# Kernel tuning notes

Measured on AMD Instinct MI355X. Metric: run time of the kernel, lower is better.

Reference implementation:

```python
import jax, jax.numpy as jnp
import numpy as np

B, M, N, HID, H, P = 16, 1024, 1024, 512, 8, 2
DH = HID // H


def setup_inputs() -> dict:
    key = jax.random.key(0)
    k1, k2, k3, k4 = jax.random.split(key, 4)
    X = jax.random.normal(k1, (B, M, HID), dtype=jnp.float32)
    Y = jax.random.normal(k2, (B, N, HID), dtype=jnp.float32)
    # learned pad prefixes (kaiming-uniform in torch; any init is fine for a numerics baseline)
    bound = np.sqrt(1.0 / HID)
    pad_x = jax.random.uniform(k3, (P, HID), dtype=jnp.float32, minval=-bound, maxval=bound)
    pad_y = jax.random.uniform(k4, (P, HID), dtype=jnp.float32, minval=-bound, maxval=bound)
    return {"X": X, "Y": Y, "pad_x": pad_x, "pad_y": pad_y}


def _project(T, pad):
    # prepend learned pad rows, split into heads -> [B, H, L+P, DH]
    b = T.shape[0]
    T = jnp.concatenate([jnp.broadcast_to(pad[None], (b, P, HID)), T], axis=1)
    return T.reshape(b, T.shape[1], H, DH).transpose(0, 2, 1, 3)


def reference(X, Y, pad_x, pad_y):
    Xp = _project(X, pad_x)  # [B,H,Mp,DH], query=key=value
    Yp = _project(Y, pad_y)  # [B,H,Np,DH]
    # shared similarity matrix (no 1/sqrt(d) scaling in the original)
    sim = jnp.einsum('bhmd,bhnd->bhmn', Xp, Yp)  # [B,H,Mp,Np]
    # masks in the original are all-ones (pad rows + torch.ones), so masked_fill is a no-op
    attn_X_by_Y = jax.nn.softmax(sim, axis=2)  # softmax over Mp (rows)
    attn_Y_by_X = jax.nn.softmax(sim, axis=3)  # softmax over Np (cols)
    # X attends in Y: attn^T @ X_value -> [B,H,Np,DH]
    X_in_Y = jnp.einsum('bhmn,bhmd->bhnd', attn_X_by_Y, Xp)[:, :, P:, :]
    X_in_Y = X_in_Y.transpose(0, 2, 1, 3).reshape(X.shape[0], -1, HID)  # [B,N,HID]
    # Y attends in X: attn @ Y_value -> [B,H,Mp,DH]
    Y_in_X = jnp.einsum('bhmn,bhnd->bhmd', attn_Y_by_X, Yp)[:, :, P:, :]
    Y_in_X = Y_in_X.transpose(0, 2, 1, 3).reshape(Y.shape[0], -1, HID)  # [B,M,HID]
    return X_in_Y, Y_in_X
```

## Files before the change

### kernel.cpp

```cpp
#include <hip/hip_runtime.h>
#include <hip/hip_bf16.h>
#include <stdint.h>

typedef _Float16 f16x8_t  __attribute__((ext_vector_type(8)));
typedef float    f32x16_t __attribute__((ext_vector_type(16)));
typedef short    s16x8_t  __attribute__((ext_vector_type(8)));
typedef unsigned uint2v   __attribute__((ext_vector_type(2)));
typedef unsigned int u32;

#define MFMA32 __builtin_amdgcn_mfma_f32_32x32x16_f16

#if __has_builtin(__builtin_amdgcn_exp2f)
#define EXP2(x) __builtin_amdgcn_exp2f(x)
#else
#define EXP2(x) exp2f(x)
#endif

__device__ __forceinline__ u32 PKRTZ(float a, float b) {
    return __builtin_bit_cast(u32, __builtin_amdgcn_cvt_pkrtz(a, b));
}

__device__ __forceinline__ void PLSWAP(u32& a, u32& b) {
#if __has_builtin(__builtin_amdgcn_permlane32_swap)
    uint2v r = __builtin_amdgcn_permlane32_swap(a, b, false, false);
    a = r[0]; b = r[1];
#else
    u32 pa = (u32)__shfl_xor((int)a, 32);
    u32 pb = (u32)__shfl_xor((int)b, 32);
    const int hi_ = (int)((threadIdx.x & 63) >> 5);
    u32 na = hi_ ? pb : a;
    u32 nb = hi_ ? b  : pa;
    a = na; b = nb;
#endif
}
__device__ __forceinline__ float swap_add(float v) {
    u32 a = __builtin_bit_cast(u32, v), b = a;
    PLSWAP(a, b);
    return __builtin_bit_cast(float, a) + __builtin_bit_cast(float, b);
}
__device__ __forceinline__ float swap_max(float v) {
    u32 a = __builtin_bit_cast(u32, v), b = a;
    PLSWAP(a, b);
    return fmaxf(__builtin_bit_cast(float, a), __builtin_bit_cast(float, b));
}

constexpr int Bb   = 16;
constexpr int HIDc = 512;
constexpr int SEQc = 1024;

constexpr int QT = 128;
constexpr int KT = 64;
constexpr int NTILES = SEQc / KT;

constexpr float LOG2E_F = 1.4426950408889634f;
constexpr float DTHR    = 11.5f;

constexpr int ROWB       = 144;
constexpr int VT_OFF     = 64 * ROWB;
constexpr int BUF_STRIDE = 2 * VT_OFF;
constexpr int LDS_TOTAL  = 2 * BUF_STRIDE;

__global__ __launch_bounds__(256, 4)
void xattn_kernel(const float* __restrict__ X, const float* __restrict__ Y,
                  const float* __restrict__ padx, const float* __restrict__ pady,
                  float* __restrict__ out)
{
    __shared__ __align__(16) unsigned char pool[LDS_TOTAL];

    const int tid  = threadIdx.x;
    const int w    = tid >> 6;
    const int lane = tid & 63;
    const int l31  = lane & 31;
    const int hi   = lane >> 5;

    const unsigned hid = blockIdx.x + gridDim.x * (blockIdx.y + gridDim.y * blockIdx.z);
    const unsigned lid = (hid & 7u) * 256u + (hid >> 3);
    const int qt   = lid & 7;
    const int bh   = (lid >> 3) & 127;
    const int pass = lid >> 10;
    const int b    = bh >> 3;
    const int h    = bh & 7;

    const float* Qp   = pass == 0 ? X : Y;
    const float* KVp  = pass == 0 ? Y : X;
    const float* padp = pass == 0 ? pady : padx;
    float* outp = out + (pass == 0 ? (size_t)Bb * SEQc * HIDc : (size_t)0);

    const float* qrow = Qp + ((size_t)b * SEQc + qt * QT + w * 32 + l31) * HIDc + h * 64;
    f16x8_t qf[4];
#pragma unroll
    for (int ds = 0; ds < 4; ++ds) {
        const float* src = qrow + ds * 16 + hi * 8;
        float4 a = *(const float4*)src;
        float4 c = *(const float4*)(src + 4);
        uint4 uu = {PKRTZ(a.x * LOG2E_F, a.y * LOG2E_F), PKRTZ(a.z * LOG2E_F, a.w * LOG2E_F),
                    PKRTZ(c.x * LOG2E_F, c.y * LOG2E_F), PKRTZ(c.z * LOG2E_F, c.w * LOG2E_F)};
        qf[ds] = __builtin_bit_cast(f16x8_t, uu);
    }

    const float* padh = padp + h * 64;
    float s0 = 0.f, s1 = 0.f;
#pragma unroll
    for (int ds = 0; ds < 4; ++ds)
#pragma unroll
        for (int j = 0; j < 8; ++j) {
            float qv = (float)qf[ds][j];
            int d = ds * 16 + hi * 8 + j;
            s0 += qv * padh[d];
            s1 += qv * padh[HIDc + d];
        }
    s0 = swap_add(s0);
    s1 = swap_add(s1);
    float mr = fmaxf(s0, s1);
    float e0 = EXP2(s0 - mr), e1 = EXP2(s1 - mr);
    float lr = e0 + e1;

    f32x16_t Oacc[2];
#pragma unroll
    for (int db = 0; db < 2; ++db)
#pragma unroll
        for (int r = 0; r < 16; ++r) {
            int d = db * 32 + (r & 3) + 8 * (r >> 2) + 4 * hi;
            Oacc[db][r] = e0 * padh[d] + e1 * padh[HIDc + d];
        }

    const unsigned key  = (unsigned)(((l31 >> 3) & 3) << 4);
    const unsigned rowb = (unsigned)(l31 * ROWB);
    unsigned kcol[4], vcol[4];
#pragma unroll
    for (int s = 0; s < 4; ++s) {
        kcol[s] = (unsigned)((s * 32 + hi * 16) ^ key);
        vcol[s] = (unsigned)(VT_OFF + ((s * 32 + hi * 16) ^ key));
    }

    const int tr = tid >> 3, tc = tid & 7;
    const float* ksrc = KVp + ((size_t)b * SEQc + 2 * tr) * HIDc + h * 64 + tc * 8;
    const unsigned kw  = (unsigned)((2 * tr) * ROWB + ((tc * 16) ^ ((((2 * tr) >> 3) & 3) << 4)));
    const unsigned vtw = (unsigned)(VT_OFF + (tc * 8) * ROWB + ((4 * tr) ^ ((tc & 3) << 4)));

    auto loadtile = [&](int idx, float4& a0, float4& a1, float4& c0, float4& c1) {
        const float* srow = ksrc + (size_t)idx * KT * HIDc;
        a0 = *(const float4*)srow;          a1 = *(const float4*)(srow + 4);
        c0 = *(const float4*)(srow + HIDc); c1 = *(const float4*)(srow + HIDc + 4);
    };
    auto stage_write = [&](int bo, const float4& a0, const float4& a1,
                           const float4& c0, const float4& c1) {
        uint4 k0 = {PKRTZ(a0.x, a0.y), PKRTZ(a0.z, a0.w), PKRTZ(a1.x, a1.y), PKRTZ(a1.z, a1.w)};
        uint4 k1 = {PKRTZ(c0.x, c0.y), PKRTZ(c0.z, c0.w), PKRTZ(c1.x, c1.y), PKRTZ(c1.z, c1.w)};
        *(uint4*)(pool + bo + kw) = k0;
        *(uint4*)(pool + bo + kw + ROWB) = k1;
        float fa[8] = {a0.x, a0.y, a0.z, a0.w, a1.x, a1.y, a1.z, a1.w};
        float fc[8] = {c0.x, c0.y, c0.z, c0.w, c1.x, c1.y, c1.z, c1.w};
#pragma unroll
        for (int j = 0; j < 8; ++j)
            *(u32*)(pool + bo + vtw + j * ROWB) = PKRTZ(fa[j], fc[j]);
    };

    auto compute = [&](int bo) {
        f32x16_t sa[2];
#pragma unroll
        for (int nb = 0; nb < 2; ++nb)
#pragma unroll
            for (int r = 0; r < 16; ++r) sa[nb][r] = 0.f;
        __builtin_amdgcn_s_setprio(1);
#pragma unroll
        for (int ds = 0; ds < 4; ++ds) {
            s16x8_t k0 = *(const s16x8_t*)(pool + bo + rowb + kcol[ds]);
            s16x8_t k1 = *(const s16x8_t*)(pool + bo + rowb + kcol[ds] + 32 * ROWB);
            sa[0] = MFMA32(__builtin_bit_cast(f16x8_t, k0), qf[ds], sa[0], 0, 0, 0);
            sa[1] = MFMA32(__builtin_bit_cast(f16x8_t, k1), qf[ds], sa[1], 0, 0, 0);
        }
        __builtin_amdgcn_s_setprio(0);

        float pm = sa[0][0];
#pragma unroll
        for (int nb = 0; nb < 2; ++nb)
#pragma unroll
            for (int r = 0; r < 16; ++r) pm = fmaxf(pm, sa[nb][r]);
        pm = swap_max(pm);
        if (!__all(pm <= mr + DTHR)) {
            float mn = fmaxf(mr, pm);
            float corr = EXP2(mr - mn);
            mr = mn;
            lr *= corr;
#pragma unroll
            for (int db = 0; db < 2; ++db)
#pragma unroll
                for (int r = 0; r < 16; ++r) Oacc[db][r] *= corr;
        }
        float pe[2][16];
        float ps = 0.f;
#pragma unroll
        for (int nb = 0; nb < 2; ++nb)
#pragma unroll
            for (int r = 0; r < 16; ++r) {
                pe[nb][r] = EXP2(sa[nb][r] - mr);
                ps += pe[nb][r];
            }
        lr += swap_add(ps);

        __builtin_amdgcn_s_setprio(1);
#pragma unroll
        for (int nb = 0; nb < 2; ++nb)
#pragma unroll
            for (int ksl = 0; ksl < 2; ++ksl) {
                u32 w0 = PKRTZ(pe[nb][8 * ksl + 0], pe[nb][8 * ksl + 1]);
                u32 w1 = PKRTZ(pe[nb][8 * ksl + 2], pe[nb][8 * ksl + 3]);
                u32 w2 = PKRTZ(pe[nb][8 * ksl + 4], pe[nb][8 * ksl + 5]);
                u32 w3 = PKRTZ(pe[nb][8 * ksl + 6], pe[nb][8 * ksl + 7]);
                PLSWAP(w0, w2);
                PLSWAP(w1, w3);
                uint4 pu = {w0, w1, w2, w3};
                f16x8_t pfrag = __builtin_bit_cast(f16x8_t, pu);
                const int ks = nb * 2 + ksl;
                s16x8_t v0 = *(const s16x8_t*)(pool + bo + rowb + vcol[ks]);
                s16x8_t v1 = *(const s16x8_t*)(pool + bo + rowb + vcol[ks] + 32 * ROWB);
                Oacc[0] = MFMA32(__builtin_bit_cast(f16x8_t, v0), pfrag, Oacc[0], 0, 0, 0);
                Oacc[1] = MFMA32(__builtin_bit_cast(f16x8_t, v1), pfrag, Oacc[1], 0, 0, 0);
            }
        __builtin_amdgcn_s_setprio(0);
    };

    {
        float4 a0, a1, c0, c1;
        loadtile(0, a0, a1, c0, c1);
        stage_write(0, a0, a1, c0, c1);
    }
    __syncthreads();
    for (int kt = 0; kt < NTILES; kt += 2) {
        {
            compute(0);
            float4 a0, a1, c0, c1;
            loadtile(kt + 1, a0, a1, c0, c1);
            stage_write(BUF_STRIDE, a0, a1, c0, c1);
            __syncthreads();
        }
        {
            compute(BUF_STRIDE);
            if (kt + 2 < NTILES) {
                float4 a0, a1, c0, c1;
                loadtile(kt + 2, a0, a1, c0, c1);
                stage_write(0, a0, a1, c0, c1);
            }
            __syncthreads();
        }
    }

    {
        const float inv = 1.0f / lr;
        float* fp = (float*)pool;
#pragma unroll
        for (int db = 0; db < 2; ++db)
#pragma unroll
            for (int r = 0; r < 16; ++r) {
                int d = db * 32 + (r & 3) + 8 * (r >> 2) + 4 * hi;
                fp[(w * 32 + l31) * 68 + d] = Oacc[db][r] * inv;
            }
    }
    __syncthreads();
    {
        const int row = tid >> 1, ch = tid & 1;
        const float* srcp = (const float*)pool + row * 68 + ch * 32;
        float* dst = outp + ((size_t)b * SEQc + qt * QT + row) * HIDc + h * 64 + ch * 32;
#pragma unroll
        for (int k = 0; k < 8; ++k)
            *(float4*)(dst + k * 4) = *(const float4*)(srcp + k * 4);
    }
}

extern "C" void kernel_launch(void* const* d_in, const int* in_sizes, int n_in,
                              void* d_out, int out_size, void* d_ws, size_t ws_size,
                              hipStream_t stream) {
    const float* X    = (const float*)d_in[0];
    const float* Y    = (const float*)d_in[1];
    const float* padx = (const float*)d_in[2];
    const float* pady = (const float*)d_in[3];
    float* out = (float*)d_out;
    (void)in_sizes; (void)n_in; (void)out_size; (void)d_ws; (void)ws_size;

    dim3 grid(SEQc / QT, Bb * 8, 2);
    hipLaunchKernelGGL(xattn_kernel, grid, dim3(256), 0, stream, X, Y, padx, pady, out);
}
```

Measured before the change: 107.7 us.

## Widen V-transpose LDS swizzle and interleave exp with PV MFMAs

Widens the XOR swizzle on the transposed-V shared-memory tile from a 2-bit to a 3-bit key, and applies the matching XOR (0x40) when reading the second half. This is meant to cut LDS bank conflicts on both the V transpose writes and the fragment reads. It also computes the exponentials inside the PV MFMA loop instead of in a separate pass, so exp work can overlap matrix ops and fewer registers stay live. The row-sum reduction moves to after the loop. The swizzle change must match on the write and read sides exactly, or results will be wrong.

```diff
diff --git a/kernel.cpp b/kernel.cpp
--- a/kernel.cpp
+++ b/kernel.cpp
@@ -124,19 +124,20 @@
             Oacc[db][r] = e0 * padh[d] + e1 * padh[HIDc + d];
         }
 
-    const unsigned key  = (unsigned)(((l31 >> 3) & 3) << 4);
+    const unsigned kkey = (unsigned)(((l31 >> 3) & 3) << 4);
+    const unsigned vkey = (unsigned)((l31 >> 3) << 4);
     const unsigned rowb = (unsigned)(l31 * ROWB);
     unsigned kcol[4], vcol[4];
 #pragma unroll
     for (int s = 0; s < 4; ++s) {
-        kcol[s] = (unsigned)((s * 32 + hi * 16) ^ key);
-        vcol[s] = (unsigned)(VT_OFF + ((s * 32 + hi * 16) ^ key));
+        kcol[s] = (unsigned)((s * 32 + hi * 16) ^ kkey);
+        vcol[s] = (unsigned)(VT_OFF + ((s * 32 + hi * 16) ^ vkey));
     }
 
     const int tr = tid >> 3, tc = tid & 7;
     const float* ksrc = KVp + ((size_t)b * SEQc + 2 * tr) * HIDc + h * 64 + tc * 8;
     const unsigned kw  = (unsigned)((2 * tr) * ROWB + ((tc * 16) ^ ((((2 * tr) >> 3) & 3) << 4)));
-    const unsigned vtw = (unsigned)(VT_OFF + (tc * 8) * ROWB + ((4 * tr) ^ ((tc & 3) << 4)));
+    const unsigned vtw = (unsigned)(VT_OFF + (tc * 8) * ROWB + ((4 * tr) ^ (tc << 4)));
 
     auto loadtile = [&](int idx, float4& a0, float4& a1, float4& c0, float4& c1) {
         const float* srow = ksrc + (size_t)idx * KT * HIDc;
@@ -188,37 +189,38 @@
 #pragma unroll
                 for (int r = 0; r < 16; ++r) Oacc[db][r] *= corr;
         }
-        float pe[2][16];
+
         float ps = 0.f;
+        __builtin_amdgcn_s_setprio(1);
 #pragma unroll
         for (int nb = 0; nb < 2; ++nb)
 #pragma unroll
-            for (int r = 0; r < 16; ++r) {
-                pe[nb][r] = EXP2(sa[nb][r] - mr);
-                ps += pe[nb][r];
-            }
-        lr += swap_add(ps);
-
-        __builtin_amdgcn_s_setprio(1);
-#pragma unroll
-        for (int nb = 0; nb < 2; ++nb)
-#pragma unroll
             for (int ksl = 0; ksl < 2; ++ksl) {
-                u32 w0 = PKRTZ(pe[nb][8 * ksl + 0], pe[nb][8 * ksl + 1]);
-                u32 w1 = PKRTZ(pe[nb][8 * ksl + 2], pe[nb][8 * ksl + 3]);
-                u32 w2 = PKRTZ(pe[nb][8 * ksl + 4], pe[nb][8 * ksl + 5]);
-                u32 w3 = PKRTZ(pe[nb][8 * ksl + 6], pe[nb][8 * ksl + 7]);
+                float x0 = EXP2(sa[nb][8 * ksl + 0] - mr);
+                float x1 = EXP2(sa[nb][8 * ksl + 1] - mr);
+                float x2 = EXP2(sa[nb][8 * ksl + 2] - mr);
+                float x3 = EXP2(sa[nb][8 * ksl + 3] - mr);
+                float x4 = EXP2(sa[nb][8 * ksl + 4] - mr);
+                float x5 = EXP2(sa[nb][8 * ksl + 5] - mr);
+                float x6 = EXP2(sa[nb][8 * ksl + 6] - mr);
+                float x7 = EXP2(sa[nb][8 * ksl + 7] - mr);
+                ps += ((x0 + x1) + (x2 + x3)) + ((x4 + x5) + (x6 + x7));
+                u32 w0 = PKRTZ(x0, x1);
+                u32 w1 = PKRTZ(x2, x3);
+                u32 w2 = PKRTZ(x4, x5);
+                u32 w3 = PKRTZ(x6, x7);
                 PLSWAP(w0, w2);
                 PLSWAP(w1, w3);
                 uint4 pu = {w0, w1, w2, w3};
                 f16x8_t pfrag = __builtin_bit_cast(f16x8_t, pu);
                 const int ks = nb * 2 + ksl;
                 s16x8_t v0 = *(const s16x8_t*)(pool + bo + rowb + vcol[ks]);
-                s16x8_t v1 = *(const s16x8_t*)(pool + bo + rowb + vcol[ks] + 32 * ROWB);
+                s16x8_t v1 = *(const s16x8_t*)(pool + bo + rowb + (vcol[ks] ^ 0x40u) + 32 * ROWB);
                 Oacc[0] = MFMA32(__builtin_bit_cast(f16x8_t, v0), pfrag, Oacc[0], 0, 0, 0);
                 Oacc[1] = MFMA32(__builtin_bit_cast(f16x8_t, v1), pfrag, Oacc[1], 0, 0, 0);
             }
         __builtin_amdgcn_s_setprio(0);
+        lr += swap_add(ps);
     };
 
     {
```

Measured after the change: 106.1 us (median of 3 runs). Within noise of the previous version (-1.4%).
